# Kernel tuning notes

Hardware: AMD Instinct MI355X
Metric: run time of the kernel (lower is better)

The kernel has to match this reference:

```python
import jax, jax.numpy as jnp
import numpy as np

K = 16          # NUM_PARTS (foreground parts); K+1 prototypes incl. background
D = 768         # EMBED_DIM
C = 200         # NUM_CLASSES
LN_EPS = 1e-6


def setup_inputs() -> dict:
    key = jax.random.key(0)
    k1, k2, k3, k4 = jax.random.split(key, 4)
    B, H, W = 32, 24, 24
    patch_features = jax.random.normal(k1, (B, H, W, D), dtype=jnp.float32)
    prototypes = 0.02 * jax.random.normal(k2, (K + 1, D), dtype=jnp.float32)
    ln_gamma = jnp.ones((D,), dtype=jnp.float32)
    ln_beta = jnp.zeros((D,), dtype=jnp.float32)
    # keras Dense default: glorot_uniform kernel, zero bias
    lim = np.sqrt(6.0 / (D + C)).astype(np.float32)
    w_cls = jax.random.uniform(k3, (D, C), dtype=jnp.float32, minval=-lim, maxval=lim)
    b_cls = jnp.zeros((C,), dtype=jnp.float32)
    return {
        "patch_features": patch_features,
        "prototypes": prototypes,
        "ln_gamma": ln_gamma,
        "ln_beta": ln_beta,
        "w_cls": w_cls,
        "b_cls": b_cls,
    }


def reference(patch_features, prototypes, ln_gamma, ln_beta, w_cls, b_cls):
    B, H, W, Dm = patch_features.shape
    P = H * W
    x = patch_features.reshape(B, P, Dm)                      # (B,P,D)

    # squared euclidean distance to K+1 prototypes, expressed as a GEMM:
    # ||z - p||^2 = ||z||^2 - 2 z.p + ||p||^2   -> (B,P,K+1)
    x_sq = jnp.sum(x * x, axis=-1, keepdims=True)             # (B,P,1)
    p_sq = jnp.sum(prototypes * prototypes, axis=-1)          # (K+1,)
    xp = jnp.einsum("bpd,kd->bpk", x, prototypes)             # (B,P,K+1)
    dists = x_sq - 2.0 * xp + p_sq                            # (B,P,K+1)

    # eval path: plain softmax over -distances
    a = jax.nn.softmax(-dists, axis=-1)                       # (B,P,K+1)

    # attention maps (B, K+1, H, W)
    A = jnp.transpose(a, (0, 2, 1)).reshape(B, K + 1, H, W)

    # weighted aggregation of patch features per part, normalized by P
    v_all = jnp.einsum("bpk,bpd->bkd", a, x) / jnp.float32(P) # (B,K+1,D)
    v_fg = v_all[:, :K, :]                                    # (B,K,D)

    # layernorm over last axis (eps=1e-6, learnable gamma/beta)
    mu = jnp.mean(v_fg, axis=-1, keepdims=True)
    var = jnp.mean(jnp.square(v_fg - mu), axis=-1, keepdims=True)
    v_norm = (v_fg - mu) * jax.lax.rsqrt(var + LN_EPS) * ln_gamma + ln_beta

    # shared per-part classifier + mean aggregation over parts
    logits_parts = jnp.einsum("bkd,dc->bkc", v_norm, w_cls) + b_cls  # (B,K,C)
    logits_agg = jnp.mean(logits_parts, axis=1)                      # (B,C)

    return (A, v_norm, logits_parts, logits_agg)
```

## Files before the change

### kernel.cpp

```cpp
#include <hip/hip_runtime.h>
#include <hip/hip_bf16.h>

#define B    32
#define P    576
#define D    768
#define K1   17
#define KFG  16
#define C    200
#define LN_EPS 1e-6f

typedef __attribute__((ext_vector_type(8))) short short8;
typedef __attribute__((ext_vector_type(4))) float f32x4;

__device__ inline short8 cvt8(float4 a, float4 b) {
    union { unsigned u[4]; short8 s; } r;
    union { __hip_bfloat162 h; unsigned u; } c;
    c.h = __float22bfloat162_rn(make_float2(a.x, a.y)); r.u[0] = c.u;
    c.h = __float22bfloat162_rn(make_float2(a.z, a.w)); r.u[1] = c.u;
    c.h = __float22bfloat162_rn(make_float2(b.x, b.y)); r.u[2] = c.u;
    c.h = __float22bfloat162_rn(make_float2(b.z, b.w)); r.u[3] = c.u;
    return r.s;
}
__device__ inline float sq8(float4 a, float4 b) {
    return a.x*a.x + a.y*a.y + a.z*a.z + a.w*a.w
         + b.x*b.x + b.y*b.y + b.z*b.z + b.w*b.w;
}

__global__ __launch_bounds__(256) void k_dots(const float* __restrict__ x,
                                              const float* __restrict__ proto,
                                              float* __restrict__ A_out,
                                              float* __restrict__ apool) {
    __shared__ float scL[4 * 64 * 11];
    const int tile = blockIdx.x, b = blockIdx.y;
    const int t = threadIdx.x, wv = t >> 6, lane = t & 63;
    const int n = lane & 15, kq = lane >> 4;
    const int p0 = tile * 16;

    const float* arow = x     + ((size_t)(b * P + p0 + n)) * D + wv * 192 + kq * 8;
    const float* brow = proto + (size_t)n  * D + wv * 192 + kq * 8;
    const float* brw6 = proto + (size_t)16 * D + wv * 192 + kq * 8;

    f32x4 acc0 = {0.f, 0.f, 0.f, 0.f};
    f32x4 acc1 = {0.f, 0.f, 0.f, 0.f};
    float sq0 = 0.f, sq6 = 0.f;

    #pragma unroll
    for (int s = 0; s < 6; ++s) {
        float4 a0 = *(const float4*)(arow + s * 32);
        float4 a1 = *(const float4*)(arow + s * 32 + 4);
        float4 b0 = *(const float4*)(brow + s * 32);
        float4 b1 = *(const float4*)(brow + s * 32 + 4);
        float4 c0 = *(const float4*)(brw6 + s * 32);
        float4 c1 = *(const float4*)(brw6 + s * 32 + 4);
        short8 A  = cvt8(a0, a1);
        short8 Bv = cvt8(b0, b1);
        short8 B6 = cvt8(c0, c1);
        sq0 += sq8(b0, b1);
        sq6 += sq8(c0, c1);
        acc0 = __builtin_amdgcn_mfma_f32_16x16x32_bf16(A, Bv, acc0, 0, 0, 0);
        acc1 = __builtin_amdgcn_mfma_f32_16x16x32_bf16(A, B6, acc1, 0, 0, 0);
    }
    sq0 += __shfl_xor(sq0, 16, 64); sq0 += __shfl_xor(sq0, 32, 64);
    sq6 += __shfl_xor(sq6, 16, 64); sq6 += __shfl_xor(sq6, 32, 64);

    {
        float* s = scL + (wv * 64 + lane) * 11;
        #pragma unroll
        for (int r = 0; r < 4; ++r) { s[r] = acc0[r]; s[r + 4] = acc1[r]; }
        s[8] = sq0; s[9] = sq6;
    }
    __syncthreads();
    if (wv != 0) return;

    float f0[4], f1[4]; float fsq0 = 0.f, fsq6 = 0.f;
    #pragma unroll
    for (int r = 0; r < 4; ++r) { f0[r] = 0.f; f1[r] = 0.f; }
    #pragma unroll
    for (int w = 0; w < 4; ++w) {
        const float* s = scL + (w * 64 + lane) * 11;
        #pragma unroll
        for (int r = 0; r < 4; ++r) { f0[r] += s[r]; f1[r] += s[r + 4]; }
        fsq0 += s[8]; fsq6 += s[9];
    }

    float a_[4], a16[4];
    #pragma unroll
    for (int r = 0; r < 4; ++r) {
        float l0  = 2.f * f0[r] - fsq0;
        float l16 = 2.f * f1[r] - fsq6;
        float mx = l0;
        #pragma unroll
        for (int o = 1; o < 16; o <<= 1) mx = fmaxf(mx, __shfl_xor(mx, o, 64));
        mx = fmaxf(mx, l16);
        float e0  = __expf(l0 - mx);
        float e16 = __expf(l16 - mx);
        float sum = e0;
        #pragma unroll
        for (int o = 1; o < 16; o <<= 1) sum += __shfl_xor(sum, o, 64);
        sum += e16;
        const float inv = 1.f / sum;
        a_[r]  = e0 * inv;
        a16[r] = e16 * inv;
    }

    *(float4*)(A_out + ((size_t)b * K1 + n) * P + p0 + kq * 4) =
        make_float4(a_[0], a_[1], a_[2], a_[3]);
    if (n == 0)
        *(float4*)(A_out + ((size_t)b * K1 + 16) * P + p0 + kq * 4) =
            make_float4(a16[0], a16[1], a16[2], a16[3]);

    const float invP = 1.f / (float)P;
    #pragma unroll
    for (int r = 0; r < 4; ++r)
        apool[((size_t)b * P + p0 + kq * 4 + r) * KFG + n] = a_[r] * invP;
}

__global__ __launch_bounds__(256, 4) void k_pool(const float* __restrict__ x,
                                                 const float* __restrict__ apool,
                                                 float* __restrict__ vpart) {
    const int dc = blockIdx.x, psl = blockIdx.y, b = blockIdx.z;
    const int t = threadIdx.x;
    const int d = dc * 256 + t;

    const float* aw = apool + ((size_t)b * P + psl * 96) * KFG;
    const float* xp = x + ((size_t)b * P + psl * 96) * D + d;

    float acc[KFG];
    #pragma unroll
    for (int k = 0; k < KFG; ++k) acc[k] = 0.f;

    #pragma unroll 4
    for (int p = 0; p < 96; ++p) {
        float xv = xp[(size_t)p * D];
        f32x4 A0 = *(const f32x4*)(aw + p * 16);
        f32x4 A1 = *(const f32x4*)(aw + p * 16 + 4);
        f32x4 A2 = *(const f32x4*)(aw + p * 16 + 8);
        f32x4 A3 = *(const f32x4*)(aw + p * 16 + 12);
        acc[0]  += A0[0] * xv; acc[1]  += A0[1] * xv; acc[2]  += A0[2] * xv; acc[3]  += A0[3] * xv;
        acc[4]  += A1[0] * xv; acc[5]  += A1[1] * xv; acc[6]  += A1[2] * xv; acc[7]  += A1[3] * xv;
        acc[8]  += A2[0] * xv; acc[9]  += A2[1] * xv; acc[10] += A2[2] * xv; acc[11] += A2[3] * xv;
        acc[12] += A3[0] * xv; acc[13] += A3[1] * xv; acc[14] += A3[2] * xv; acc[15] += A3[3] * xv;
    }
    float* o = vpart + ((size_t)(psl * B + b) * KFG) * D + d;
    #pragma unroll
    for (int k = 0; k < KFG; ++k) o[(size_t)k * D] = acc[k];
}

__global__ __launch_bounds__(256) void k_ln(const float* __restrict__ vpart,
                                            const float* __restrict__ gamma,
                                            const float* __restrict__ beta,
                                            float* __restrict__ vnorm_out,
                                            float* __restrict__ vT) {
    const int k = blockIdx.x, b = blockIdx.y, t = threadIdx.x;
    const int lane = t & 63, wv = t >> 6;

    float v[3]; float s1 = 0.f, s2 = 0.f;
    #pragma unroll
    for (int j = 0; j < 3; ++j) {
        const int d = t + j * 256;
        float s = 0.f;
        #pragma unroll
        for (int psl = 0; psl < 6; ++psl)
            s += vpart[((size_t)(psl * B + b) * KFG + k) * D + d];
        v[j] = s; s1 += s; s2 += s * s;
    }
    #pragma unroll
    for (int o = 1; o < 64; o <<= 1) {
        s1 += __shfl_xor(s1, o, 64);
        s2 += __shfl_xor(s2, o, 64);
    }
    __shared__ float r1[4], r2[4];
    if (lane == 0) { r1[wv] = s1; r2[wv] = s2; }
    __syncthreads();
    s1 = r1[0] + r1[1] + r1[2] + r1[3];
    s2 = r2[0] + r2[1] + r2[2] + r2[3];

    const float mean = s1 * (1.f / (float)D);
    const float var  = s2 * (1.f / (float)D) - mean * mean;
    const float rs   = rsqrtf(var + LN_EPS);

    #pragma unroll
    for (int j = 0; j < 3; ++j) {
        const int d = t + j * 256;
        float vn = (v[j] - mean) * rs * gamma[d] + beta[d];
        vnorm_out[((size_t)b * KFG + k) * D + d] = vn;
        vT[((size_t)b * D + d) * KFG + k] = vn;
    }
}

__global__ __launch_bounds__(256) void k_cls(const float* __restrict__ vT,
                                             const float* __restrict__ W,
                                             float* __restrict__ lpart) {
    const int dq = blockIdx.x, b = blockIdx.y;
    const int c = threadIdx.x;
    const int cc = c < C ? c : (C - 1);

    const float* vt = vT + ((size_t)b * D + dq * 48) * KFG;
    const float* Wp = W + (size_t)dq * 48 * C + cc;

    float acc[KFG];
    #pragma unroll
    for (int k = 0; k < KFG; ++k) acc[k] = 0.f;

    #pragma unroll 4
    for (int i = 0; i < 48; ++i) {
        float wl = Wp[(size_t)i * C];
        f32x4 V0 = *(const f32x4*)(vt + i * 16);
        f32x4 V1 = *(const f32x4*)(vt + i * 16 + 4);
        f32x4 V2 = *(const f32x4*)(vt + i * 16 + 8);
        f32x4 V3 = *(const f32x4*)(vt + i * 16 + 12);
        acc[0]  += V0[0] * wl; acc[1]  += V0[1] * wl; acc[2]  += V0[2] * wl; acc[3]  += V0[3] * wl;
        acc[4]  += V1[0] * wl; acc[5]  += V1[1] * wl; acc[6]  += V1[2] * wl; acc[7]  += V1[3] * wl;
        acc[8]  += V2[0] * wl; acc[9]  += V2[1] * wl; acc[10] += V2[2] * wl; acc[11] += V2[3] * wl;
        acc[12] += V3[0] * wl; acc[13] += V3[1] * wl; acc[14] += V3[2] * wl; acc[15] += V3[3] * wl;
    }
    if (c < C) {
        float* o = lpart + ((size_t)(dq * B + b) * KFG) * C + c;
        #pragma unroll
        for (int k = 0; k < KFG; ++k) o[(size_t)k * C] = acc[k];
    }
}

__global__ __launch_bounds__(256) void k_comb(const float* __restrict__ lpart,
                                              const float* __restrict__ bcls,
                                              float* __restrict__ parts,
                                              float* __restrict__ agg) {
    const int b = blockIdx.x, c = threadIdx.x;
    if (c >= C) return;
    const float bc = bcls[c];
    float s_agg = 0.f;
    #pragma unroll
    for (int k = 0; k < KFG; ++k) {
        float s = bc;
        #pragma unroll
        for (int dq = 0; dq < 16; ++dq)
            s += lpart[((size_t)(dq * B + b) * KFG + k) * C + c];
        parts[((size_t)b * KFG + k) * C + c] = s;
        s_agg += s;
    }
    agg[(size_t)b * C + c] = s_agg * (1.f / (float)KFG);
}

extern "C" void kernel_launch(void* const* d_in, const int* in_sizes, int n_in,
                              void* d_out, int out_size, void* d_ws, size_t ws_size,
                              hipStream_t stream) {
    const float* x     = (const float*)d_in[0];
    const float* proto = (const float*)d_in[1];
    const float* gamma = (const float*)d_in[2];
    const float* beta  = (const float*)d_in[3];
    const float* W     = (const float*)d_in[4];
    const float* bcls  = (const float*)d_in[5];

    float* out = (float*)d_out;
    float* A_out     = out;
    float* vnorm_out = out + 313344;
    float* parts_out = out + 706560;
    float* agg_out   = out + 808960;

    float* ws = (float*)d_ws;
    float* apool = ws;
    float* vpart = apool + 294912;
    float* vT    = vpart + 2359296;
    float* lpart = vT + 393216;

    hipLaunchKernelGGL(k_dots, dim3(36, B),   dim3(256), 0, stream, x, proto, A_out, apool);
    hipLaunchKernelGGL(k_pool, dim3(3, 6, B), dim3(256), 0, stream, x, apool, vpart);
    hipLaunchKernelGGL(k_ln,   dim3(KFG, B),  dim3(256), 0, stream, vpart, gamma, beta, vnorm_out, vT);
    hipLaunchKernelGGL(k_cls,  dim3(16, B),   dim3(256), 0, stream, vT, W, lpart);
    hipLaunchKernelGGL(k_comb, dim3(B),       dim3(256), 0, stream, lpart, bcls, parts_out, agg_out);
}
```

Measured before the change: 153.4 us.

## Fuse layernorm, classifier and part-mean into one per-batch kernel

Replaces the separate layernorm, split-D classifier and combine kernels with one 1024-thread block per batch. The block sums the partial pools, computes layernorm statistics for all 16 parts, keeps the normalized vectors in LDS and runs the full D=768 classifier reduction in-block, writing part logits and their mean directly. This drops two launches and the vT and lpart workspace round trips. In exchange it runs only 32 blocks, and each classifier thread walks a serial 768-step loop, which leaves much of the GPU idle.

```diff
diff --git a/kernel.cpp b/kernel.cpp
--- a/kernel.cpp
+++ b/kernel.cpp
@@ -146,99 +146,101 @@
     for (int k = 0; k < KFG; ++k) o[(size_t)k * D] = acc[k];
 }
 
-__global__ __launch_bounds__(256) void k_ln(const float* __restrict__ vpart,
-                                            const float* __restrict__ gamma,
-                                            const float* __restrict__ beta,
-                                            float* __restrict__ vnorm_out,
-                                            float* __restrict__ vT) {
-    const int k = blockIdx.x, b = blockIdx.y, t = threadIdx.x;
+__global__ __launch_bounds__(1024) void k_lncls(const float* __restrict__ vpart,
+                                                const float* __restrict__ gamma,
+                                                const float* __restrict__ beta,
+                                                const float* __restrict__ W,
+                                                const float* __restrict__ bcls,
+                                                float* __restrict__ vnorm_out,
+                                                float* __restrict__ parts,
+                                                float* __restrict__ agg) {
+    const int b = blockIdx.x;
+    const int t = threadIdx.x;
     const int lane = t & 63, wv = t >> 6;
 
-    float v[3]; float s1 = 0.f, s2 = 0.f;
-    #pragma unroll
-    for (int j = 0; j < 3; ++j) {
-        const int d = t + j * 256;
-        float s = 0.f;
-        #pragma unroll
-        for (int psl = 0; psl < 6; ++psl)
-            s += vpart[((size_t)(psl * B + b) * KFG + k) * D + d];
-        v[j] = s; s1 += s; s2 += s * s;
-    }
-    #pragma unroll
-    for (int o = 1; o < 64; o <<= 1) {
-        s1 += __shfl_xor(s1, o, 64);
-        s2 += __shfl_xor(s2, o, 64);
-    }
-    __shared__ float r1[4], r2[4];
-    if (lane == 0) { r1[wv] = s1; r2[wv] = s2; }
-    __syncthreads();
-    s1 = r1[0] + r1[1] + r1[2] + r1[3];
-    s2 = r2[0] + r2[1] + r2[2] + r2[3];
-
-    const float mean = s1 * (1.f / (float)D);
-    const float var  = s2 * (1.f / (float)D) - mean * mean;
-    const float rs   = rsqrtf(var + LN_EPS);
-
-    #pragma unroll
-    for (int j = 0; j < 3; ++j) {
-        const int d = t + j * 256;
-        float vn = (v[j] - mean) * rs * gamma[d] + beta[d];
-        vnorm_out[((size_t)b * KFG + k) * D + d] = vn;
-        vT[((size_t)b * D + d) * KFG + k] = vn;
-    }
-}
-
-__global__ __launch_bounds__(256) void k_cls(const float* __restrict__ vT,
-                                             const float* __restrict__ W,
-                                             float* __restrict__ lpart) {
-    const int dq = blockIdx.x, b = blockIdx.y;
-    const int c = threadIdx.x;
+    __shared__ __attribute__((aligned(16))) float vn_lds[D][20];
+    __shared__ float r1[KFG][12], r2[KFG][12];
+    __shared__ float2 mrs[KFG];
+    __shared__ float sagg[4][256];
+
+    const bool act = t < D;
+    float v[KFG];
+
+    if (act) {
+        const int d = t;
+        #pragma unroll
+        for (int k = 0; k < KFG; ++k) {
+            float s = 0.f;
+            #pragma unroll
+            for (int q = 0; q < 6; ++q)
+                s += vpart[((size_t)(q * B + b) * KFG + k) * D + d];
+            v[k] = s;
+        }
+        #pragma unroll
+        for (int k = 0; k < KFG; ++k) {
+            float s1 = v[k], s2 = v[k] * v[k];
+            #pragma unroll
+            for (int o = 1; o < 64; o <<= 1) {
+                s1 += __shfl_xor(s1, o, 64);
+                s2 += __shfl_xor(s2, o, 64);
+            }
+            if (lane == 0) { r1[k][wv] = s1; r2[k][wv] = s2; }
+        }
+    }
+    __syncthreads();
+    if (t < KFG) {
+        float s1 = 0.f, s2 = 0.f;
+        #pragma unroll
+        for (int w = 0; w < 12; ++w) { s1 += r1[t][w]; s2 += r2[t][w]; }
+        const float mean = s1 * (1.f / (float)D);
+        const float var  = s2 * (1.f / (float)D) - mean * mean;
+        mrs[t] = make_float2(mean, rsqrtf(var + LN_EPS));
+    }
+    __syncthreads();
+    if (act) {
+        const int d = t;
+        const float g = gamma[d], be = beta[d];
+        #pragma unroll
+        for (int j = 0; j < 4; ++j) {
+            f32x4 q;
+            #pragma unroll
+            for (int i = 0; i < 4; ++i) {
+                const int k = j * 4 + i;
+                const float2 m = mrs[k];
+                const float vn = (v[k] - m.x) * m.y * g + be;
+                q[i] = vn;
+                vnorm_out[((size_t)b * KFG + k) * D + d] = vn;
+            }
+            *(f32x4*)&vn_lds[d][j * 4] = q;
+        }
+    }
+    __syncthreads();
+
+    const int kg = t >> 8, c = t & 255;
     const int cc = c < C ? c : (C - 1);
-
-    const float* vt = vT + ((size_t)b * D + dq * 48) * KFG;
-    const float* Wp = W + (size_t)dq * 48 * C + cc;
-
-    float acc[KFG];
-    #pragma unroll
-    for (int k = 0; k < KFG; ++k) acc[k] = 0.f;
-
+    const float bc = bcls[cc];
+    const float* Wp = W + cc;
+
+    float a0 = 0.f, a1 = 0.f, a2 = 0.f, a3 = 0.f;
     #pragma unroll 4
-    for (int i = 0; i < 48; ++i) {
-        float wl = Wp[(size_t)i * C];
-        f32x4 V0 = *(const f32x4*)(vt + i * 16);
-        f32x4 V1 = *(const f32x4*)(vt + i * 16 + 4);
-        f32x4 V2 = *(const f32x4*)(vt + i * 16 + 8);
-        f32x4 V3 = *(const f32x4*)(vt + i * 16 + 12);
-        acc[0]  += V0[0] * wl; acc[1]  += V0[1] * wl; acc[2]  += V0[2] * wl; acc[3]  += V0[3] * wl;
-        acc[4]  += V1[0] * wl; acc[5]  += V1[1] * wl; acc[6]  += V1[2] * wl; acc[7]  += V1[3] * wl;
-        acc[8]  += V2[0] * wl; acc[9]  += V2[1] * wl; acc[10] += V2[2] * wl; acc[11] += V2[3] * wl;
-        acc[12] += V3[0] * wl; acc[13] += V3[1] * wl; acc[14] += V3[2] * wl; acc[15] += V3[3] * wl;
-    }
+    for (int d = 0; d < D; ++d) {
+        const float wl = Wp[(size_t)d * C];
+        const f32x4 vq = *(const f32x4*)&vn_lds[d][kg * 4];
+        a0 += vq[0] * wl; a1 += vq[1] * wl; a2 += vq[2] * wl; a3 += vq[3] * wl;
+    }
+    const float s0 = a0 + bc, s1 = a1 + bc, s2 = a2 + bc, s3 = a3 + bc;
     if (c < C) {
-        float* o = lpart + ((size_t)(dq * B + b) * KFG) * C + c;
-        #pragma unroll
-        for (int k = 0; k < KFG; ++k) o[(size_t)k * C] = acc[k];
-    }
-}
-
-__global__ __launch_bounds__(256) void k_comb(const float* __restrict__ lpart,
-                                              const float* __restrict__ bcls,
-                                              float* __restrict__ parts,
-                                              float* __restrict__ agg) {
-    const int b = blockIdx.x, c = threadIdx.x;
-    if (c >= C) return;
-    const float bc = bcls[c];
-    float s_agg = 0.f;
-    #pragma unroll
-    for (int k = 0; k < KFG; ++k) {
-        float s = bc;
-        #pragma unroll
-        for (int dq = 0; dq < 16; ++dq)
-            s += lpart[((size_t)(dq * B + b) * KFG + k) * C + c];
-        parts[((size_t)b * KFG + k) * C + c] = s;
-        s_agg += s;
-    }
-    agg[(size_t)b * C + c] = s_agg * (1.f / (float)KFG);
+        float* o = parts + ((size_t)b * KFG + kg * 4) * C + c;
+        o[0]         = s0;
+        o[(size_t)C] = s1;
+        o[2*(size_t)C] = s2;
+        o[3*(size_t)C] = s3;
+        sagg[kg][c] = s0 + s1 + s2 + s3;
+    }
+    __syncthreads();
+    if (kg == 0 && c < C)
+        agg[(size_t)b * C + c] =
+            (sagg[0][c] + sagg[1][c] + sagg[2][c] + sagg[3][c]) * (1.f / (float)KFG);
 }
 
 extern "C" void kernel_launch(void* const* d_in, const int* in_sizes, int n_in,
@@ -260,12 +262,9 @@
     float* ws = (float*)d_ws;
     float* apool = ws;
     float* vpart = apool + 294912;
-    float* vT    = vpart + 2359296;
-    float* lpart = vT + 393216;
-
-    hipLaunchKernelGGL(k_dots, dim3(36, B),   dim3(256), 0, stream, x, proto, A_out, apool);
-    hipLaunchKernelGGL(k_pool, dim3(3, 6, B), dim3(256), 0, stream, x, apool, vpart);
-    hipLaunchKernelGGL(k_ln,   dim3(KFG, B),  dim3(256), 0, stream, vpart, gamma, beta, vnorm_out, vT);
-    hipLaunchKernelGGL(k_cls,  dim3(16, B),   dim3(256), 0, stream, vT, W, lpart);
-    hipLaunchKernelGGL(k_comb, dim3(B),       dim3(256), 0, stream, lpart, bcls, parts_out, agg_out);
-}
+
+    hipLaunchKernelGGL(k_dots,  dim3(36, B),   dim3(256),  0, stream, x, proto, A_out, apool);
+    hipLaunchKernelGGL(k_pool,  dim3(3, 6, B), dim3(256),  0, stream, x, apool, vpart);
+    hipLaunchKernelGGL(k_lncls, dim3(B),       dim3(1024), 0, stream, vpart, gamma, beta, W, bcls,
+                       vnorm_out, parts_out, agg_out);
+}
```

Result: slower. 183.5 us (+19.6%).
